# Kernel optimization log

Hardware: AMD Instinct MI355X
Metric: run time of the kernel (lower is better)

## Reference

```python
import jax, jax.numpy as jnp
import numpy as np

B, T, D, DE, S, P = 16384, 2, 1024, 512, 4, 4  # batch, tasks, inp_dim, expt_dim, share, specific


def setup_inputs() -> dict:
    key = jax.random.key(0)
    ks = jax.random.split(key, 8)
    sc = 0.02
    return {
        "x0": jax.random.normal(ks[0], (B, D), jnp.float32),
        "x1": jax.random.normal(ks[1], (B, D), jnp.float32),
        "W_share": jax.random.normal(ks[2], (S, D, DE), jnp.float32) * sc,
        "b_share": jnp.zeros((S, DE), jnp.float32),
        "W_spcf": jax.random.normal(ks[3], (T, P, D, DE), jnp.float32) * sc,
        "b_spcf": jnp.zeros((T, P, DE), jnp.float32),
        "W_gate": jax.random.normal(ks[4], (T, D, S + P), jnp.float32) * sc,
        "b_gate": jnp.zeros((T, S + P), jnp.float32),
    }


def reference(x0, x1, W_share, b_share, W_spcf, b_spcf, W_gate, b_gate):
    # cat_x: [B, T, D]
    x = jnp.stack([x0, x1], axis=1)
    # per-task gate over all S+P experts: [B, T, S+P]
    gates = jax.nn.softmax(jnp.einsum("btd,tde->bte", x, W_gate) + b_gate, axis=-1)
    # shared experts applied to every task's input: [B, T, S, DE]
    share = jax.nn.relu(jnp.einsum("btd,sdf->btsf", x, W_share) + b_share[None, None])
    # task-specific experts applied to their own task input: [B, T, P, DE]
    spcf = jax.nn.relu(jnp.einsum("btd,tpdf->btpf", x, W_spcf) + b_spcf[None])
    experts = jnp.concatenate([share, spcf], axis=2)  # [B, T, S+P, DE]
    # softmax-gated mixture: [B, T, DE] (== list of per-task [B, DE] in the original)
    return jnp.einsum("bte,btef->btf", gates, experts)
```

## Files before the change

### kernel.cpp

```cpp
#include <hip/hip_runtime.h>
#include <stdint.h>

#define kB  16384
#define kD  1024
#define kDE 512

typedef __bf16 bf16x8 __attribute__((ext_vector_type(8)));
typedef float  f32x4  __attribute__((ext_vector_type(4)));

__device__ __forceinline__ unsigned short f2bf(float f) {
    union { float f; unsigned u; } v; v.f = f;
    unsigned r = v.u + 0x7FFFu + ((v.u >> 16) & 1u);
    return (unsigned short)(r >> 16);
}

__device__ __forceinline__ void async16(unsigned short* lds, const unsigned short* g) {
    __builtin_amdgcn_global_load_lds(
        (const __attribute__((address_space(1))) unsigned int*)g,
        (__attribute__((address_space(3))) unsigned int*)lds, 16, 0, 0);
}

__global__ __launch_bounds__(256) void prep_all(
    const float* __restrict__ Wsh, const float* __restrict__ Wsp,
    unsigned short* __restrict__ Wt,
    const float* __restrict__ x0, const float* __restrict__ x1,
    const float* __restrict__ Wg, const float* __restrict__ bg,
    unsigned short* __restrict__ xb, float* __restrict__ g) {
    if (blockIdx.x < 1536) {
        __shared__ float tile[64][65];
        const int idx = blockIdx.x;
        const int slot = idx >> 7;
        const int rem = idx & 127;
        const int k0 = (rem & 15) * 64;
        const int n0 = (rem >> 4) * 64;
        const float* src = (slot < 4) ? (Wsh + (size_t)slot * kD * kDE)
                                      : (Wsp + (size_t)(slot - 4) * kD * kDE);
        const int tid = threadIdx.x;
        const int lr = tid >> 4, lc = (tid & 15) * 4;
#pragma unroll
        for (int i = 0; i < 4; i++) {
            const float4 v = *(const float4*)&src[(size_t)(k0 + lr + i * 16) * kDE + n0 + lc];
            tile[lr + i * 16][lc + 0] = v.x;
            tile[lr + i * 16][lc + 1] = v.y;
            tile[lr + i * 16][lc + 2] = v.z;
            tile[lr + i * 16][lc + 3] = v.w;
        }
        __syncthreads();
        const int wn = tid >> 2, wk = (tid & 3) * 16;
        unsigned short* dst = Wt + (size_t)slot * kDE * kD + (size_t)(n0 + wn) * kD + k0 + wk;
#pragma unroll
        for (int j = 0; j < 4; j++) {
            ushort4 h;
            h.x = f2bf(tile[wk + j * 4 + 0][wn]);
            h.y = f2bf(tile[wk + j * 4 + 1][wn]);
            h.z = f2bf(tile[wk + j * 4 + 2][wn]);
            h.w = f2bf(tile[wk + j * 4 + 3][wn]);
            *(ushort4*)(dst + j * 4) = h;
        }
        return;
    }
    const int wid = threadIdx.x >> 6, lane = threadIdx.x & 63;
    const int r = (blockIdx.x - 1536) * 4 + wid;
    const int t = r >> 14, b = r & 16383;
    const float* xrow = (t ? x1 : x0) + (size_t)b * kD;
    unsigned short* xbrow = xb + (size_t)(t * kB + b) * kD;
    const float* Wgt = Wg + t * kD * 8;
    float p[8] = {0.f,0.f,0.f,0.f,0.f,0.f,0.f,0.f};
#pragma unroll
    for (int it = 0; it < 4; it++) {
        const int d0 = it * 256 + lane * 4;
        const float4 v = *(const float4*)(xrow + d0);
        ushort4 h;
        h.x = f2bf(v.x); h.y = f2bf(v.y); h.z = f2bf(v.z); h.w = f2bf(v.w);
        *(ushort4*)(xbrow + d0) = h;
        const float xv[4] = {v.x, v.y, v.z, v.w};
#pragma unroll
        for (int j = 0; j < 4; j++) {
            const float* wrow = Wgt + (size_t)(d0 + j) * 8;
            const float4 wa = *(const float4*)wrow;
            const float4 wb = *(const float4*)(wrow + 4);
            p[0] += xv[j] * wa.x; p[1] += xv[j] * wa.y;
            p[2] += xv[j] * wa.z; p[3] += xv[j] * wa.w;
            p[4] += xv[j] * wb.x; p[5] += xv[j] * wb.y;
            p[6] += xv[j] * wb.z; p[7] += xv[j] * wb.w;
        }
    }
#pragma unroll
    for (int e = 0; e < 8; e++) {
        float v = p[e];
#pragma unroll
        for (int s = 1; s < 64; s <<= 1) v += __shfl_xor(v, s, 64);
        p[e] = v;
    }
    float lg[8];
#pragma unroll
    for (int e = 0; e < 8; e++) lg[e] = p[e] + bg[t * 8 + e];
    float mx = lg[0];
#pragma unroll
    for (int e = 1; e < 8; e++) mx = fmaxf(mx, lg[e]);
    float s = 0.f;
#pragma unroll
    for (int e = 0; e < 8; e++) { lg[e] = __expf(lg[e] - mx); s += lg[e]; }
    const float inv = 1.f / s;
    if (lane == 0) {
        float* gp = g + (size_t)(t * kB + b) * 8;
        float4 g0 = {lg[0]*inv, lg[1]*inv, lg[2]*inv, lg[3]*inv};
        float4 g1 = {lg[4]*inv, lg[5]*inv, lg[6]*inv, lg[7]*inv};
        *(float4*)gp = g0;
        *(float4*)(gp + 4) = g1;
    }
}

__global__ __launch_bounds__(512, 2) void moe_gemm(
    const unsigned short* __restrict__ xb, const unsigned short* __restrict__ Wt,
    const float* __restrict__ g, const float* __restrict__ bsh,
    const float* __restrict__ bsp, float* __restrict__ out) {
    __shared__ __align__(16) unsigned short As[2][128 * 64];
    __shared__ __align__(16) unsigned short Bs[2][8 * 64 * 64];

    const int bid = blockIdx.x;
    const int swz = (bid & 7) * 256 + (bid >> 3);
    const int ct = swz & 7;
    const int rt = (swz >> 3) & 127;
    const int t  = swz >> 10;
    const int n0 = ct * 64;

    const int tid = threadIdx.x, wid = tid >> 6, lane = tid & 63;
    const int wr = wid >> 2, wc = wid & 3;
    const bool early = (wid < 4);

    const int swzChunk = ((lane & 7) ^ ((lane >> 3) & 7)) * 8;
    const unsigned short* aSrc = xb + (size_t)t * kB * kD +
        (size_t)(rt * 128 + wid * 16 + (lane >> 3)) * kD + swzChunk;
    const int slot = (wid < 4) ? wid : (4 + t * 4 + (wid - 4));
    const unsigned short* bSrc = Wt + (size_t)slot * kDE * kD +
        (size_t)(n0 + (lane >> 3)) * kD + swzChunk;

    const int rAbase = (wr * 64 + (lane & 15)) * 64;
    const int bOff   = (wc * 16 + (lane & 15)) * 64;
    const int lx     = lane & 7;
    const int kg     = lane >> 4;

    f32x4 acc[8][4];
#pragma unroll
    for (int e = 0; e < 8; e++)
#pragma unroll
        for (int m = 0; m < 4; m++) acc[e][m] = (f32x4){0.f, 0.f, 0.f, 0.f};

    bf16x8 af[4], bfr[4];

#define S_A(buf, ktn)                                                          \
    async16(&As[buf][wid * 1024 + 0 * 512], aSrc + (ktn) * 64 + 0 * 8 * kD);   \
    async16(&As[buf][wid * 1024 + 1 * 512], aSrc + (ktn) * 64 + 1 * 8 * kD);

#define S_B(buf, ktn, j)                                                       \
    async16(&Bs[buf][wid * 4096 + (j) * 512], bSrc + (ktn) * 64 + (j) * 8 * kD);

#define R_A(buf, ks)                                                           \
    _Pragma("unroll")                                                          \
    for (int m = 0; m < 4; m++)                                                \
        af[m] = *(const bf16x8*)&As[buf][rAbase + m * 1024 +                   \
                                         ((((ks) * 4 + kg) ^ lx) << 3)];

#define R_B4(buf, ks, e0)                                                      \
    _Pragma("unroll")                                                          \
    for (int i = 0; i < 4; i++)                                                \
        bfr[i] = *(const bf16x8*)&Bs[buf][((e0) + i) * 4096 + bOff +           \
                                          ((((ks) * 4 + kg) ^ lx) << 3)];

#define MM4(e0)                                                                \
    asm volatile("s_waitcnt lgkmcnt(0)" ::: "memory");                         \
    __builtin_amdgcn_sched_barrier(0);                                         \
    __builtin_amdgcn_s_setprio(1);                                             \
    _Pragma("unroll")                                                          \
    for (int i = 0; i < 4; i++)                                                \
        _Pragma("unroll")                                                      \
        for (int m = 0; m < 4; m++)                                            \
            acc[(e0) + i][m] = __builtin_amdgcn_mfma_f32_16x16x32_bf16(        \
                af[m], bfr[i], acc[(e0) + i][m], 0, 0, 0);                     \
    __builtin_amdgcn_s_setprio(0);

#define STEP(cur, nxt, ktn)                                                    \
    {                                                                          \
                                                            \
        R_A(cur, 0); R_B4(cur, 0, 0);                                          \
        if (early) {                                                           \
            S_A(nxt, ktn); S_B(nxt, ktn, 0); S_B(nxt, ktn, 1);                 \
        } else {                                                               \
            S_A(nxt, ktn);                                                     \
            asm volatile("s_waitcnt vmcnt(2)" ::: "memory");                   \
        }                                                                      \
        __builtin_amdgcn_s_barrier();                                          \
        MM4(0);                                                                \
                                                \
        R_B4(cur, 0, 4);                                                       \
        if (early) {                                                           \
            S_B(nxt, ktn, 2); S_B(nxt, ktn, 3);                                \
            S_B(nxt, ktn, 4); S_B(nxt, ktn, 5);                                \
        }                                                                      \
        __builtin_amdgcn_s_barrier();                                          \
        MM4(4);                                                                \
                                                            \
        R_A(cur, 1); R_B4(cur, 1, 0);                                          \
        if (early) {                                                           \
            S_B(nxt, ktn, 6); S_B(nxt, ktn, 7);                                \
        } else {                                                               \
            S_B(nxt, ktn, 0); S_B(nxt, ktn, 1);                                \
            S_B(nxt, ktn, 2); S_B(nxt, ktn, 3);                                \
        }                                                                      \
        __builtin_amdgcn_s_barrier();                                          \
        MM4(0);                                                                \
                      \
        R_B4(cur, 1, 4);                                                       \
        if (!early) {                                                          \
            S_B(nxt, ktn, 4); S_B(nxt, ktn, 5);                                \
            S_B(nxt, ktn, 6); S_B(nxt, ktn, 7);                                \
        }                                                                      \
        __builtin_amdgcn_s_barrier();                                          \
        MM4(4);                                                                \
        if (early) { asm volatile("s_waitcnt vmcnt(0)" ::: "memory"); }        \
        else       { asm volatile("s_waitcnt vmcnt(8)" ::: "memory"); }        \
        __builtin_amdgcn_s_barrier();                                          \
    }

    S_A(0, 0);
    S_B(0, 0, 0); S_B(0, 0, 1); S_B(0, 0, 2); S_B(0, 0, 3);
    S_B(0, 0, 4); S_B(0, 0, 5); S_B(0, 0, 6); S_B(0, 0, 7);
    if (early) { asm volatile("s_waitcnt vmcnt(0)" ::: "memory"); }
    else       { asm volatile("s_waitcnt vmcnt(8)" ::: "memory"); }
    __builtin_amdgcn_s_barrier();

    for (int kt2 = 0; kt2 < 8; ++kt2) {
        STEP(0, 1, kt2 * 2 + 1)
        STEP(1, 0, (kt2 * 2 + 2) & 15)
    }
    asm volatile("s_waitcnt vmcnt(0)" ::: "memory");

#undef S_A
#undef S_B
#undef R_A
#undef R_B4
#undef MM4
#undef STEP

    const int col = n0 + wc * 16 + (lane & 15);
    float bv[8];
#pragma unroll
    for (int e = 0; e < 8; e++)
        bv[e] = (e < 4) ? bsh[e * kDE + col] : bsp[(t * 4 + (e - 4)) * kDE + col];

#pragma unroll
    for (int m = 0; m < 4; m++) {
        const int r0 = rt * 128 + wr * 64 + m * 16 + kg * 4;
#pragma unroll
        for (int q = 0; q < 4; q++) {
            const float* gp = g + ((size_t)t * kB + r0 + q) * 8;
            const float4 ga = *(const float4*)gp;
            const float4 gb = *(const float4*)(gp + 4);
            float s = ga.x * fmaxf(acc[0][m][q] + bv[0], 0.f)
                    + ga.y * fmaxf(acc[1][m][q] + bv[1], 0.f)
                    + ga.z * fmaxf(acc[2][m][q] + bv[2], 0.f)
                    + ga.w * fmaxf(acc[3][m][q] + bv[3], 0.f)
                    + gb.x * fmaxf(acc[4][m][q] + bv[4], 0.f)
                    + gb.y * fmaxf(acc[5][m][q] + bv[5], 0.f)
                    + gb.z * fmaxf(acc[6][m][q] + bv[6], 0.f)
                    + gb.w * fmaxf(acc[7][m][q] + bv[7], 0.f);
            out[((size_t)(r0 + q) * 2 + t) * kDE + col] = s;
        }
    }
}

extern "C" void kernel_launch(void* const* d_in, const int* in_sizes, int n_in,
                              void* d_out, int out_size, void* d_ws, size_t ws_size,
                              hipStream_t stream) {
    const float* x0  = (const float*)d_in[0];
    const float* x1  = (const float*)d_in[1];
    const float* Wsh = (const float*)d_in[2];
    const float* bsh = (const float*)d_in[3];
    const float* Wsp = (const float*)d_in[4];
    const float* bsp = (const float*)d_in[5];
    const float* Wg  = (const float*)d_in[6];
    const float* bg  = (const float*)d_in[7];
    float* out = (float*)d_out;

    char* ws = (char*)d_ws;
    unsigned short* xb = (unsigned short*)ws;
    unsigned short* Wt = (unsigned short*)(ws + 67108864);
    float* g  = (float*)(ws + 67108864 + 12582912);

    prep_all<<<dim3(9728), dim3(256), 0, stream>>>(Wsh, Wsp, Wt, x0, x1, Wg, bg, xb, g);
    moe_gemm<<<dim3(2048), dim3(512), 0, stream>>>(xb, Wt, g, bsh, bsp, out);
}
```

Before: 415.4 us.

## Switch GEMM main loop to triple-buffered K=32 tiles with uniform wave loading

The MoE GEMM main loop moves from double-buffered 64-wide K tiles, with asymmetric early/late wave load schedules, to triple-buffered 32-wide K tiles where every wave issues the same loads. The LDS layout and XOR swizzle are reworked for the narrower tiles, and the loop prefetches two tiles ahead with one vmcnt wait per tile. The aim is to hide global-to-LDS latency better and simplify the load schedule. In exchange there are twice as many barrier rounds per unit of K, and LDS use shrinks slightly.

```diff
diff --git a/kernel.cpp b/kernel.cpp
--- a/kernel.cpp
+++ b/kernel.cpp
@@ -115,8 +115,8 @@
     const unsigned short* __restrict__ xb, const unsigned short* __restrict__ Wt,
     const float* __restrict__ g, const float* __restrict__ bsh,
     const float* __restrict__ bsp, float* __restrict__ out) {
-    __shared__ __align__(16) unsigned short As[2][128 * 64];
-    __shared__ __align__(16) unsigned short Bs[2][8 * 64 * 64];
+    __shared__ __align__(16) unsigned short As[3][128 * 32];
+    __shared__ __align__(16) unsigned short Bs[3][8 * 64 * 32];
 
     const int bid = blockIdx.x;
     const int swz = (bid & 7) * 256 + (bid >> 3);
@@ -127,19 +127,19 @@
 
     const int tid = threadIdx.x, wid = tid >> 6, lane = tid & 63;
     const int wr = wid >> 2, wc = wid & 3;
-    const bool early = (wid < 4);
-
-    const int swzChunk = ((lane & 7) ^ ((lane >> 3) & 7)) * 8;
-    const unsigned short* aSrc = xb + (size_t)t * kB * kD +
-        (size_t)(rt * 128 + wid * 16 + (lane >> 3)) * kD + swzChunk;
+
+    const int dSt = (lane & 7) ^ (lane >> 3);
+    const unsigned short* aS = xb + (size_t)t * kB * kD +
+        (size_t)(rt * 128 + wid * 16 + (lane >> 3) * 2 + (dSt >> 2)) * kD + (dSt & 3) * 8;
     const int slot = (wid < 4) ? wid : (4 + t * 4 + (wid - 4));
-    const unsigned short* bSrc = Wt + (size_t)slot * kDE * kD +
-        (size_t)(n0 + (lane >> 3)) * kD + swzChunk;
-
-    const int rAbase = (wr * 64 + (lane & 15)) * 64;
-    const int bOff   = (wc * 16 + (lane & 15)) * 64;
-    const int lx     = lane & 7;
-    const int kg     = lane >> 4;
+    const unsigned short* bS = Wt + (size_t)slot * kDE * kD +
+        (size_t)(n0 + (lane >> 3) * 2 + (dSt >> 2)) * kD + (dSt & 3) * 8;
+
+    const int l15h = (lane & 15) >> 1;
+    const int swR = (((lane & 1) * 4 + (lane >> 4)) ^ l15h);
+    const int aRd = wr * 2048 + l15h * 64 + swR * 8;
+    const int bRd = wc * 512  + l15h * 64 + swR * 8;
+    const int kg  = lane >> 4;
 
     f32x4 acc[8][4];
 #pragma unroll
@@ -149,24 +149,19 @@
 
     bf16x8 af[4], bfr[4];
 
-#define S_A(buf, ktn)                                                          \
-    async16(&As[buf][wid * 1024 + 0 * 512], aSrc + (ktn) * 64 + 0 * 8 * kD);   \
-    async16(&As[buf][wid * 1024 + 1 * 512], aSrc + (ktn) * 64 + 1 * 8 * kD);
-
-#define S_B(buf, ktn, j)                                                       \
-    async16(&Bs[buf][wid * 4096 + (j) * 512], bSrc + (ktn) * 64 + (j) * 8 * kD);
-
-#define R_A(buf, ks)                                                           \
+#define S_A(buf, ktn)  async16(&As[buf][wid * 512], aS + (ktn) * 32);
+#define S_B(buf, ktn, j) \
+    async16(&Bs[buf][wid * 2048 + (j) * 512], bS + (size_t)(j) * 16 * kD + (ktn) * 32);
+
+#define R_A(buf)                                                               \
     _Pragma("unroll")                                                          \
     for (int m = 0; m < 4; m++)                                                \
-        af[m] = *(const bf16x8*)&As[buf][rAbase + m * 1024 +                   \
-                                         ((((ks) * 4 + kg) ^ lx) << 3)];
-
-#define R_B4(buf, ks, e0)                                                      \
+        af[m] = *(const bf16x8*)&As[buf][aRd + m * 512];
+
+#define R_B4(buf, e0)                                                          \
     _Pragma("unroll")                                                          \
     for (int i = 0; i < 4; i++)                                                \
-        bfr[i] = *(const bf16x8*)&Bs[buf][((e0) + i) * 4096 + bOff +           \
-                                          ((((ks) * 4 + kg) ^ lx) << 3)];
+        bfr[i] = *(const bf16x8*)&Bs[buf][bRd + ((e0) + i) * 2048];
 
 #define MM4(e0)                                                                \
     asm volatile("s_waitcnt lgkmcnt(0)" ::: "memory");                         \
@@ -180,68 +175,57 @@
                 af[m], bfr[i], acc[(e0) + i][m], 0, 0, 0);                     \
     __builtin_amdgcn_s_setprio(0);
 
-#define STEP(cur, nxt, ktn)                                                    \
+#define TILE(cur, stg, sTile)                                                  \
     {                                                                          \
-                                                            \
-        R_A(cur, 0); R_B4(cur, 0, 0);                                          \
-        if (early) {                                                           \
-            S_A(nxt, ktn); S_B(nxt, ktn, 0); S_B(nxt, ktn, 1);                 \
-        } else {                                                               \
-            S_A(nxt, ktn);                                                     \
-            asm volatile("s_waitcnt vmcnt(2)" ::: "memory");                   \
-        }                                                                      \
+                                                                      \
+        R_A(cur); R_B4(cur, 0);                                                \
+        S_A(stg, sTile); S_B(stg, sTile, 0); S_B(stg, sTile, 1);               \
         __builtin_amdgcn_s_barrier();                                          \
         MM4(0);                                                                \
-                                                \
-        R_B4(cur, 0, 4);                                                       \
-        if (early) {                                                           \
-            S_B(nxt, ktn, 2); S_B(nxt, ktn, 3);                                \
-            S_B(nxt, ktn, 4); S_B(nxt, ktn, 5);                                \
-        }                                                                      \
+        __builtin_amdgcn_s_barrier();                                          \
+                                                                      \
+        R_B4(cur, 4);                                                          \
+        S_B(stg, sTile, 2); S_B(stg, sTile, 3);                                \
+        asm volatile("s_waitcnt vmcnt(5)" ::: "memory");                       \
         __builtin_amdgcn_s_barrier();                                          \
         MM4(4);                                                                \
-                                                            \
-        R_A(cur, 1); R_B4(cur, 1, 0);                                          \
-        if (early) {                                                           \
-            S_B(nxt, ktn, 6); S_B(nxt, ktn, 7);                                \
-        } else {                                                               \
-            S_B(nxt, ktn, 0); S_B(nxt, ktn, 1);                                \
-            S_B(nxt, ktn, 2); S_B(nxt, ktn, 3);                                \
-        }                                                                      \
+        __builtin_amdgcn_s_barrier();                                          \
+    }
+
+#define TILE_LAST(cur)                                                         \
+    {                                                                          \
+        R_A(cur); R_B4(cur, 0);                                                \
         __builtin_amdgcn_s_barrier();                                          \
         MM4(0);                                                                \
-                      \
-        R_B4(cur, 1, 4);                                                       \
-        if (!early) {                                                          \
-            S_B(nxt, ktn, 4); S_B(nxt, ktn, 5);                                \
-            S_B(nxt, ktn, 6); S_B(nxt, ktn, 7);                                \
-        }                                                                      \
+        __builtin_amdgcn_s_barrier();                                          \
+        R_B4(cur, 4);                                                          \
+        asm volatile("s_waitcnt vmcnt(0)" ::: "memory");                       \
         __builtin_amdgcn_s_barrier();                                          \
         MM4(4);                                                                \
-        if (early) { asm volatile("s_waitcnt vmcnt(0)" ::: "memory"); }        \
-        else       { asm volatile("s_waitcnt vmcnt(8)" ::: "memory"); }        \
-        __builtin_amdgcn_s_barrier();                                          \
-    }
-
-    S_A(0, 0);
-    S_B(0, 0, 0); S_B(0, 0, 1); S_B(0, 0, 2); S_B(0, 0, 3);
-    S_B(0, 0, 4); S_B(0, 0, 5); S_B(0, 0, 6); S_B(0, 0, 7);
-    if (early) { asm volatile("s_waitcnt vmcnt(0)" ::: "memory"); }
-    else       { asm volatile("s_waitcnt vmcnt(8)" ::: "memory"); }
+        __builtin_amdgcn_s_barrier();                                          \
+    }
+
+    S_A(0, 0); S_B(0, 0, 0); S_B(0, 0, 1); S_B(0, 0, 2); S_B(0, 0, 3);
+    S_A(1, 1); S_B(1, 1, 0); S_B(1, 1, 1); S_B(1, 1, 2); S_B(1, 1, 3);
+    asm volatile("s_waitcnt vmcnt(5)" ::: "memory");
     __builtin_amdgcn_s_barrier();
 
-    for (int kt2 = 0; kt2 < 8; ++kt2) {
-        STEP(0, 1, kt2 * 2 + 1)
-        STEP(1, 0, (kt2 * 2 + 2) & 15)
-    }
-    asm volatile("s_waitcnt vmcnt(0)" ::: "memory");
+    for (int i3 = 0; i3 < 10; ++i3) {
+        const int b = i3 * 3;
+        TILE(0, 2, b + 2)
+        TILE(1, 0, b + 3)
+        TILE(2, 1, b + 4)
+    }
+    TILE_LAST(0)
+    TILE_LAST(1)
 
 #undef S_A
 #undef S_B
 #undef R_A
 #undef R_B4
 #undef MM4
-#undef STEP
+#undef TILE
+#undef TILE_LAST
 
     const int col = n0 + wc * 16 + (lane & 15);
     float bv[8];
```

After: 438.6 us. +5.6%, slower.
